# Optimization experiments

Measured on AMD Instinct MI355X. Metric: run time of the kernel, lower is better.

Reference implementation:

```python
import jax, jax.numpy as jnp
import numpy as np

N = 50000; E = 1600000; F = 128; H = 128; C = 40; G = 4
GRID = jnp.linspace(-2.0, 2.0, G)          # FastKAN default grid [-2, 2]
DENOM = 4.0 / (G - 1)                      # (grid_max - grid_min) / (num_grids - 1)
EPS = 1e-5
DIMS = [(F, H), (H, H), (F + 2 * H, C)]    # conv0, conv1, conv_out (skip concat)


def setup_inputs() -> dict:
    key = jax.random.key(0)
    ks = iter(jax.random.split(key, 64))
    inp = {}
    inp["x"] = jax.random.normal(next(ks), (N, F), jnp.float32)
    inp["edge_index"] = jax.random.randint(next(ks), (2, E), 0, N)
    for i, (di, do) in enumerate(DIMS):
        inp[f"c{i}_ln_g"] = jnp.ones((di,), jnp.float32)
        inp[f"c{i}_ln_b"] = jnp.zeros((di,), jnp.float32)
        inp[f"c{i}_sw"] = jax.random.normal(next(ks), (do, di * G), jnp.float32) * 0.1
        inp[f"c{i}_sb"] = jnp.zeros((do,), jnp.float32)
        inp[f"c{i}_bw"] = jax.random.normal(next(ks), (do, di), jnp.float32) * (1.0 / np.sqrt(di))
        inp[f"c{i}_bb"] = jnp.zeros((do,), jnp.float32)
        inp[f"c{i}_bias"] = jnp.zeros((do,), jnp.float32)   # GCNConv output bias
    inp["bn_g"] = jnp.ones((H,), jnp.float32)
    inp["bn_b"] = jnp.zeros((H,), jnp.float32)
    return inp


def _fkan(h, lg, lb, sw, sb, bw, bb):
    # FastKANLayer: LayerNorm -> RBF basis -> spline linear, plus SiLU base branch
    mu = h.mean(-1, keepdims=True)
    var = jnp.mean(jnp.square(h - mu), -1, keepdims=True)
    hn = (h - mu) * jax.lax.rsqrt(var + EPS) * lg + lb
    basis = jnp.exp(-jnp.square((hn[..., None] - GRID) / DENOM))  # [N, d, G]
    basis = basis.reshape(h.shape[0], -1)                          # [N, d*G]
    return basis @ sw.T + sb + jax.nn.silu(h) @ bw.T + bb


def _forward(x, edge_index, params, bn_g, bn_b):
    # gcn_norm with self-loops, symmetric normalization
    row = jnp.concatenate([edge_index[0], jnp.arange(N)])
    col = jnp.concatenate([edge_index[1], jnp.arange(N)])
    deg = jax.ops.segment_sum(jnp.ones_like(row, jnp.float32), col, num_segments=N)
    dis = jnp.where(deg > 0, jax.lax.rsqrt(jnp.maximum(deg, 1e-12)), 0.0)
    norm = dis[row] * dis[col]

    def conv(h, p):
        hw = _fkan(h, *p[:6])  # lin = FKANLayer applied before propagate
        return jax.ops.segment_sum(norm[:, None] * hw[row], col, num_segments=N) + p[6]

    def bn(h):  # BatchNorm1d, training-mode batch stats (biased var); dropout p=0
        mu = h.mean(0)
        var = jnp.mean(jnp.square(h - mu), 0)
        return (h - mu) * jax.lax.rsqrt(var + EPS) * bn_g + bn_b

    skips = [x]
    h = x
    for p in params[:-1]:
        h = bn(conv(h, p))
        skips.append(h)
    h = jnp.concatenate(skips, axis=1)  # skip=True
    return conv(h, params[-1])


def reference(x, edge_index, c0_ln_g, c0_ln_b, c0_sw, c0_sb, c0_bw, c0_bb, c0_bias,
              c1_ln_g, c1_ln_b, c1_sw, c1_sb, c1_bw, c1_bb, c1_bias,
              c2_ln_g, c2_ln_b, c2_sw, c2_sb, c2_bw, c2_bb, c2_bias, bn_g, bn_b):
    params = [
        (c0_ln_g, c0_ln_b, c0_sw, c0_sb, c0_bw, c0_bb, c0_bias),
        (c1_ln_g, c1_ln_b, c1_sw, c1_sb, c1_bw, c1_bb, c1_bias),
        (c2_ln_g, c2_ln_b, c2_sw, c2_sb, c2_bw, c2_bb, c2_bias),
    ]
    return _forward(x, edge_index, params, bn_g, bn_b)
```

## Files before the change

kernel.cpp:

```cpp
#include <hip/hip_runtime.h>
#include <math.h>

constexpr int NN = 50000;
constexpr int NE = 1600000;
constexpr float LN_EPS = 1e-5f;

constexpr int NBKT  = 8;
constexpr int SPAN  = NN / NBKT;
constexpr int CHUNK = 8192;
constexpr int NB1   = (NE + CHUNK - 1) / CHUNK;
constexpr int NSB   = (NN + 255) / 256;

typedef __attribute__((ext_vector_type(8))) short short8;
typedef __attribute__((ext_vector_type(4))) float f32x4;

__device__ __forceinline__ short f2bf(float f)
{
    unsigned u = __builtin_bit_cast(unsigned, f);
    u += 0x7fffu + ((u >> 16) & 1u);
    return (short)(u >> 16);
}

__device__ __forceinline__ float2 bf2x2(unsigned p)
{
    float2 r;
    r.x = __builtin_bit_cast(float, p << 16);
    r.y = __builtin_bit_cast(float, p & 0xffff0000u);
    return r;
}

__global__ __launch_bounds__(256) void csr_hist(const int* __restrict__ col,
                                                int* __restrict__ degi,
                                                int* __restrict__ histo)
{
    __shared__ int hcnt[NBKT];
    const int tid = threadIdx.x;
    if (tid < NBKT) hcnt[tid] = 0;
    __syncthreads();
    const int e0 = blockIdx.x * CHUNK;
    const int e1 = min(e0 + CHUNK, NE);
    for (int e = e0 + tid; e < e1; e += 256) {
        int c = col[e];
        atomicAdd(&degi[c], 1);
        atomicAdd(&hcnt[(unsigned)c / (unsigned)SPAN], 1);
    }
    __syncthreads();
    if (tid < NBKT) histo[tid * NB1 + blockIdx.x] = hcnt[tid];
}

__global__ __launch_bounds__(256) void csr_scan2(int* __restrict__ histo)
{
    constexpr int M = NBKT * NB1;
    constexpr int T = (M + 255) / 256;
    __shared__ int part[256];
    const int t = threadIdx.x;
    int v[T];
    int s = 0;
    #pragma unroll
    for (int j = 0; j < T; ++j) {
        int i = t * T + j;
        v[j] = (i < M) ? histo[i] : 0;
        s += v[j];
    }
    part[t] = s;
    __syncthreads();
    for (int d = 1; d < 256; d <<= 1) {
        int add = (t >= d) ? part[t - d] : 0;
        __syncthreads();
        part[t] += add;
        __syncthreads();
    }
    int run = part[t] - s;
    #pragma unroll
    for (int j = 0; j < T; ++j) {
        int i = t * T + j;
        if (i < M) { histo[i] = run; run += v[j]; }
    }
}

__global__ __launch_bounds__(256) void csr_part(const int* __restrict__ ei,
                                                const int* __restrict__ histo,
                                                uint2* __restrict__ staging)
{
    __shared__ int lcur[NBKT];
    const int tid = threadIdx.x;
    if (tid < NBKT) lcur[tid] = histo[tid * NB1 + blockIdx.x];
    __syncthreads();
    const int e0 = blockIdx.x * CHUNK;
    const int e1 = min(e0 + CHUNK, NE);
    for (int e = e0 + tid; e < e1; e += 256) {
        int r = ei[e];
        int c = ei[NE + e];
        int slot = atomicAdd(&lcur[(unsigned)c / (unsigned)SPAN], 1);
        staging[slot] = make_uint2((unsigned)r, (unsigned)c);
    }
}

template<int PB2>
__global__ __launch_bounds__(256) void csr_scatter(const uint2* __restrict__ staging,
                                                   const int* __restrict__ off,
                                                   int* __restrict__ cur,
                                                   int* __restrict__ rows)
{
    const int b   = blockIdx.x & (NBKT - 1);
    const int blk = blockIdx.x >> 3;
    const int base = off[b * SPAN];
    const int end  = off[(b + 1) * SPAN];
    for (int i = base + blk * 256 + threadIdx.x; i < end; i += PB2 * 256) {
        uint2 e = staging[i];
        int p = off[e.y] + atomicAdd(&cur[e.y], 1);
        rows[p] = (int)e.x;
    }
}

__global__ void dis_kernel(const int* __restrict__ degi, float* __restrict__ dis)
{
    int i = blockIdx.x * 256 + threadIdx.x;
    if (i < NN) dis[i] = rsqrtf((float)degi[i] + 1.0f);
}

__global__ __launch_bounds__(256) void scan_p1(const int* __restrict__ deg,
                                               int* __restrict__ off,
                                               int* __restrict__ partials)
{
    __shared__ int sh[256];
    const int t = threadIdx.x;
    const int i = blockIdx.x * 256 + t;
    int v = (i < NN) ? deg[i] : 0;
    sh[t] = v;
    __syncthreads();
    for (int d = 1; d < 256; d <<= 1) {
        int add = (t >= d) ? sh[t - d] : 0;
        __syncthreads();
        sh[t] += add;
        __syncthreads();
    }
    if (i < NN) off[i] = sh[t] - v;
    if (t == 255) partials[blockIdx.x] = sh[255];
}

__global__ __launch_bounds__(256) void scan_p2(int* __restrict__ partials)
{
    __shared__ int sh[256];
    const int t = threadIdx.x;
    int v = (t < NSB) ? partials[t] : 0;
    sh[t] = v;
    __syncthreads();
    for (int d = 1; d < 256; d <<= 1) {
        int add = (t >= d) ? sh[t - d] : 0;
        __syncthreads();
        sh[t] += add;
        __syncthreads();
    }
    if (t < NSB) partials[t] = sh[t] - v;
    if (t == 255) partials[NSB] = sh[255];
}

__global__ __launch_bounds__(256) void scan_p3(int* __restrict__ off,
                                               const int* __restrict__ partials)
{
    const int i = blockIdx.x * 256 + threadIdx.x;
    if (i < NN) off[i] += partials[blockIdx.x];
    if (i == 0) off[NN] = partials[NSB];
}

__global__ void pack_frag(const float* __restrict__ sw, const float* __restrict__ bw,
                          short* __restrict__ wtf, int D, int OT, int DO, int total)
{
    int idx = blockIdx.x * 256 + threadIdx.x;
    if (idx >= total) return;
    int j8   = idx & 7;
    int lane = (idx >> 3) & 63;
    int rest = idx >> 9;
    int ot = rest % OT, kk = rest / OT;
    int g4 = lane >> 4;
    int s  = kk * 8 + j8;
    int f  = g4 * (D / 4) + s / 5;
    int g5 = s % 5;
    int o  = ot * 16 + (lane & 15);
    float val = 0.f;
    if (o < DO) val = (g5 < 4) ? sw[o * D * 4 + f * 4 + g5] : bw[o * D + f];
    wtf[idx] = f2bf(val);
}

template<int D, int DO, int OT, int KKC, int NODES>
__global__ __launch_bounds__(NODES * 4) void fkan_reg(
    const float* __restrict__ s0, const float* __restrict__ s1, const float* __restrict__ s2,
    const float* __restrict__ ln_g, const float* __restrict__ ln_b,
    const short* __restrict__ wtf, const float* __restrict__ sb, const float* __restrict__ bb,
    short* __restrict__ out)
{
    constexpr int BW  = D / 4;
    constexpr int GBS = BW + 1;
    constexpr int RS  = 4 * GBS + 1;
    __shared__ unsigned pkL[NODES * RS];

    const int tid = threadIdx.x;

    {
        const int anode = tid >> 2, q = tid & 3;
        const int gnode = blockIdx.x * NODES + anode;
        const int snode = (gnode < NN) ? gnode : (NN - 1);
        unsigned* prow = &pkL[anode * RS + q * GBS];
        float sum = 0.f, sq = 0.f;
        #pragma unroll
        for (int i4 = 0; i4 < BW / 4; ++i4) {
            int f = q * BW + i4 * 4;
            const float* src = (D == 128) ? s0 : ((f < 128) ? s0 : (f < 256) ? s1 : s2);
            float4 v = *(const float4*)&src[snode * 128 + (f & 127)];
            sum += (v.x + v.y) + (v.z + v.w);
            sq  += (v.x * v.x + v.y * v.y) + (v.z * v.z + v.w * v.w);
            prow[i4 * 4 + 0] = __builtin_bit_cast(unsigned, v.x);
            prow[i4 * 4 + 1] = __builtin_bit_cast(unsigned, v.y);
            prow[i4 * 4 + 2] = __builtin_bit_cast(unsigned, v.z);
            prow[i4 * 4 + 3] = __builtin_bit_cast(unsigned, v.w);
        }
        sum += __shfl_xor(sum, 1); sum += __shfl_xor(sum, 2);
        sq  += __shfl_xor(sq, 1);  sq  += __shfl_xor(sq, 2);
        float mu   = sum * (1.0f / D);
        float var  = sq * (1.0f / D) - mu * mu;
        float rstd = rsqrtf(var + LN_EPS);
        #pragma unroll 4
        for (int i = 0; i < BW; ++i) {
            int f = q * BW + i;
            float v  = __builtin_bit_cast(float, prow[i]);
            float hn = (v - mu) * rstd * ln_g[f] + ln_b[f];
            float sl = v / (1.0f + __expf(-v));
            prow[i] = ((unsigned)(unsigned short)f2bf(hn) << 16)
                    | ((unsigned)(unsigned short)f2bf(sl) & 0xffffu);
        }
    }
    __syncthreads();

    const int wv = tid >> 6, lane = tid & 63;
    const int m = lane & 15, g4 = lane >> 4;
    const unsigned* pkb = &pkL[(wv * 16 + m) * RS + g4 * GBS];

    f32x4 acc[OT];
    #pragma unroll
    for (int ot = 0; ot < OT; ++ot) acc[ot] = f32x4{0.f, 0.f, 0.f, 0.f};

    union AU { unsigned u[4]; short8 s; };

    for (int per = 0; per < KKC / 5; ++per) {
        const unsigned* pp = pkb + per * 8;
        const short* bp = wtf + ((per * 5) * OT * 512) + lane * 8;
        #pragma unroll
        for (int c = 0; c < 5; ++c) {
            unsigned p[3];
            float h75[3];
            constexpr int FL0[5] = {0, 1, 3, 4, 6};
            constexpr int NF[5]  = {2, 3, 2, 3, 2};
            #pragma unroll
            for (int i = 0; i < 3; ++i) {
                if (i < NF[c]) {
                    p[i] = pp[FL0[c] + i];
                    h75[i] = __builtin_bit_cast(float, p[i] & 0xffff0000u) * 0.75f;
                }
            }
            AU a;
            #pragma unroll
            for (int i = 0; i < 4; ++i) {
                unsigned v2[2];
                #pragma unroll
                for (int h = 0; h < 2; ++h) {
                    int sl = c * 8 + 2 * i + h;
                    int fl = sl / 5 - FL0[c];
                    int g  = sl % 5;
                    if (g == 4) {
                        v2[h] = p[fl] & 0xffffu;
                    } else {
                        float t = h75[fl] + (1.5f - (float)g);
                        float e = __expf(-t * t);
                        v2[h] = (unsigned)(unsigned short)f2bf(e);
                    }
                }
                a.u[i] = (v2[0] & 0xffffu) | (v2[1] << 16);
            }
            #pragma unroll
            for (int ot = 0; ot < OT; ++ot) {
                short8 b = *(const short8*)(bp + (c * OT + ot) * 512);
                acc[ot] = __builtin_amdgcn_mfma_f32_16x16x32_bf16(a.s, b, acc[ot], 0, 0, 0);
            }
        }
    }

    const int nrow0 = blockIdx.x * NODES + wv * 16 + g4 * 4;
    #pragma unroll
    for (int ot = 0; ot < OT; ++ot) {
        int o = ot * 16 + m;
        if (o < DO) {
            float cb = sb[o] + bb[o];
            #pragma unroll
            for (int r = 0; r < 4; ++r) {
                int nr = nrow0 + r;
                if (nr < NN) out[nr * DO + o] = f2bf(acc[ot][r] + cb);
            }
        }
    }
}

template<int DO>
__global__ __launch_bounds__(64) void agg_gather_bf16(
    const int* __restrict__ off, const int* __restrict__ rows,
    const float* __restrict__ dis, const short* __restrict__ hwb,
    const float* __restrict__ bias, float* __restrict__ out)
{
    constexpr int ACT = DO / 2;
    const int n   = blockIdx.x;
    const int tid = threadIdx.x;
    __shared__ int   srow[64];
    __shared__ float swgt[64];

    const int e0 = off[n], e1 = off[n + 1];
    const float dn = dis[n];
    float ax = 0.f, ay = 0.f;
    if (tid < ACT) {
        unsigned p = *(const unsigned*)&hwb[n * DO + 2 * tid];
        float2 v = bf2x2(p);
        ax = dn * dn * v.x + bias[2 * tid];
        ay = dn * dn * v.y + bias[2 * tid + 1];
    }

    for (int t0 = e0; t0 < e1; t0 += 64) {
        const int nt = min(64, e1 - t0);
        if (tid < nt) {
            int r = rows[t0 + tid];
            srow[tid] = r;
            swgt[tid] = dn * dis[r];
        }
        __syncthreads();
        if (tid < ACT) {
            #pragma unroll 4
            for (int j = 0; j < nt; ++j) {
                unsigned p = *(const unsigned*)&hwb[srow[j] * DO + 2 * tid];
                float2 v = bf2x2(p);
                float w = swgt[j];
                ax += w * v.x;
                ay += w * v.y;
            }
        }
        __syncthreads();
    }
    if (tid < ACT) {
        out[n * DO + 2 * tid]     = ax;
        out[n * DO + 2 * tid + 1] = ay;
    }
}

__global__ void bn_stats(const float* __restrict__ h, float* __restrict__ stats)
{
    __shared__ float s1[256], s2[256];
    int c = threadIdx.x & 127;
    int half = threadIdx.x >> 7;
    float sum = 0.f, sq = 0.f;
    for (int n = blockIdx.x * 2 + half; n < NN; n += 512) {
        float v = h[n * 128 + c];
        sum += v; sq += v * v;
    }
    s1[threadIdx.x] = sum; s2[threadIdx.x] = sq;
    __syncthreads();
    if (half == 0) {
        s1[c] += s1[c + 128]; s2[c] += s2[c + 128];
        atomicAdd(&stats[c],        s1[c]);
        atomicAdd(&stats[c + 128],  s2[c]);
    }
}

__global__ void bn_apply(float* __restrict__ h, const float* __restrict__ stats,
                         const float* __restrict__ g, const float* __restrict__ b)
{
    int idx = blockIdx.x * 256 + threadIdx.x;
    if (idx >= NN * 128) return;
    int c = idx & 127;
    float mu  = stats[c] * (1.0f / NN);
    float var = stats[c + 128] * (1.0f / NN) - mu * mu;
    h[idx] = (h[idx] - mu) * rsqrtf(var + LN_EPS) * g[c] + b[c];
}

extern "C" void kernel_launch(void* const* d_in, const int* in_sizes, int n_in,
                              void* d_out, int out_size, void* d_ws, size_t ws_size,
                              hipStream_t stream)
{
    auto F = [&](int i) { return (const float*)d_in[i]; };
    const float* x  = F(0);
    const int*   ei = (const int*)d_in[1];
    const float* bn_g = F(23);
    const float* bn_b = F(24);

    short* wtf0 = (short*)d_ws;
    short* wtf1 = wtf0 + 81920;
    short* wtf2 = wtf1 + 81920;
    short* hwb  = wtf2 + 92160;
    float* dis  = (float*)(hwb + 6400000);
    float* h1   = dis + 50000;
    float* h2   = h1  + 6400000;
    float* stats = h2 + 6400000;
    int*   degi = (int*)(stats + 256);
    int*   off  = degi + 50000;
    int*   cur  = off + 50001;
    int*   rows = cur + 50000;
    int*   histo = rows + NE;
    int*   partials = histo + NBKT * NB1;
    uint2* staging = (uint2*)h1;
    float* outf = (float*)d_out;

    (void)hipMemsetAsync(degi, 0, 50000 * sizeof(int), stream);
    (void)hipMemsetAsync(cur,  0, 50000 * sizeof(int), stream);
    csr_hist<<<NB1, 256, 0, stream>>>(ei + NE, degi, histo);
    dis_kernel<<<(NN + 255) / 256, 256, 0, stream>>>(degi, dis);
    scan_p1<<<NSB, 256, 0, stream>>>(degi, off, partials);
    scan_p2<<<1, 256, 0, stream>>>(partials);
    scan_p3<<<NSB, 256, 0, stream>>>(off, partials);
    csr_scan2<<<1, 256, 0, stream>>>(histo);
    csr_part<<<NB1, 256, 0, stream>>>(ei, histo, staging);
    csr_scatter<128><<<128 * NBKT, 256, 0, stream>>>(staging, off, cur, rows);

    pack_frag<<<(81920 + 255) / 256, 256, 0, stream>>>(F(4),  F(6),  wtf0, 128, 8, 128, 81920);
    pack_frag<<<(81920 + 255) / 256, 256, 0, stream>>>(F(11), F(13), wtf1, 128, 8, 128, 81920);
    pack_frag<<<(92160 + 255) / 256, 256, 0, stream>>>(F(18), F(20), wtf2, 384, 3, 40,  92160);

    const int gridN64 = (NN + 63) / 64;
    const int gridN32 = (NN + 31) / 32;
    const int gridNF  = (NN * 128 + 255) / 256;

    fkan_reg<128, 128, 8, 20, 64><<<gridN64, 256, 0, stream>>>(x, nullptr, nullptr,
        F(2), F(3), wtf0, F(5), F(7), hwb);
    agg_gather_bf16<128><<<NN, 64, 0, stream>>>(off, rows, dis, hwb, F(8), h1);
    (void)hipMemsetAsync(stats, 0, 256 * sizeof(float), stream);
    bn_stats<<<256, 256, 0, stream>>>(h1, stats);
    bn_apply<<<gridNF, 256, 0, stream>>>(h1, stats, bn_g, bn_b);

    fkan_reg<128, 128, 8, 20, 64><<<gridN64, 256, 0, stream>>>(h1, nullptr, nullptr,
        F(9), F(10), wtf1, F(12), F(14), hwb);
    agg_gather_bf16<128><<<NN, 64, 0, stream>>>(off, rows, dis, hwb, F(15), h2);
    (void)hipMemsetAsync(stats, 0, 256 * sizeof(float), stream);
    bn_stats<<<256, 256, 0, stream>>>(h2, stats);
    bn_apply<<<gridNF, 256, 0, stream>>>(h2, stats, bn_g, bn_b);

    fkan_reg<384, 40, 3, 60, 32><<<gridN32, 128, 0, stream>>>(x, h1, h2,
        F(16), F(17), wtf2, F(19), F(21), hwb);
    agg_gather_bf16<40><<<NN, 64, 0, stream>>>(off, rows, dis, hwb, F(22), outf);
}
```

Baseline: 595.6 us.

## Chunk fkan_reg feature staging into LDS to shrink shared memory footprint

The fused LayerNorm/RBF/MFMA kernel now computes LayerNorm statistics in a first pass over global memory. It then stages packed bf16 features into shared memory in NCH chunks, with the last layer using two chunks so the LDS buffer is about half the size. The aim is higher occupancy for the D=384 layer. The cost is reading each input row twice from global memory and an extra block barrier per chunk, and ln_g/ln_b are now loaded as float4.

```diff
diff --git a/kernel.cpp b/kernel.cpp
--- a/kernel.cpp
+++ b/kernel.cpp
@@ -183,58 +183,43 @@
     wtf[idx] = f2bf(val);
 }
 
-template<int D, int DO, int OT, int KKC, int NODES>
+template<int D, int DO, int OT, int KKC, int NODES, int NCH>
 __global__ __launch_bounds__(NODES * 4) void fkan_reg(
     const float* __restrict__ s0, const float* __restrict__ s1, const float* __restrict__ s2,
     const float* __restrict__ ln_g, const float* __restrict__ ln_b,
     const short* __restrict__ wtf, const float* __restrict__ sb, const float* __restrict__ bb,
     short* __restrict__ out)
 {
-    constexpr int BW  = D / 4;
-    constexpr int GBS = BW + 1;
-    constexpr int RS  = 4 * GBS + 1;
+    constexpr int BW   = D / 4;
+    constexpr int CW   = BW / NCH;
+    constexpr int GBS  = CW + 1;
+    constexpr int RS   = 4 * GBS + 1;
+    constexpr int PPC  = (KKC / NCH) / 5;
     __shared__ unsigned pkL[NODES * RS];
 
     const int tid = threadIdx.x;
-
-    {
-        const int anode = tid >> 2, q = tid & 3;
-        const int gnode = blockIdx.x * NODES + anode;
-        const int snode = (gnode < NN) ? gnode : (NN - 1);
-        unsigned* prow = &pkL[anode * RS + q * GBS];
-        float sum = 0.f, sq = 0.f;
-        #pragma unroll
-        for (int i4 = 0; i4 < BW / 4; ++i4) {
-            int f = q * BW + i4 * 4;
-            const float* src = (D == 128) ? s0 : ((f < 128) ? s0 : (f < 256) ? s1 : s2);
-            float4 v = *(const float4*)&src[snode * 128 + (f & 127)];
-            sum += (v.x + v.y) + (v.z + v.w);
-            sq  += (v.x * v.x + v.y * v.y) + (v.z * v.z + v.w * v.w);
-            prow[i4 * 4 + 0] = __builtin_bit_cast(unsigned, v.x);
-            prow[i4 * 4 + 1] = __builtin_bit_cast(unsigned, v.y);
-            prow[i4 * 4 + 2] = __builtin_bit_cast(unsigned, v.z);
-            prow[i4 * 4 + 3] = __builtin_bit_cast(unsigned, v.w);
-        }
-        sum += __shfl_xor(sum, 1); sum += __shfl_xor(sum, 2);
-        sq  += __shfl_xor(sq, 1);  sq  += __shfl_xor(sq, 2);
-        float mu   = sum * (1.0f / D);
-        float var  = sq * (1.0f / D) - mu * mu;
-        float rstd = rsqrtf(var + LN_EPS);
-        #pragma unroll 4
-        for (int i = 0; i < BW; ++i) {
-            int f = q * BW + i;
-            float v  = __builtin_bit_cast(float, prow[i]);
-            float hn = (v - mu) * rstd * ln_g[f] + ln_b[f];
-            float sl = v / (1.0f + __expf(-v));
-            prow[i] = ((unsigned)(unsigned short)f2bf(hn) << 16)
-                    | ((unsigned)(unsigned short)f2bf(sl) & 0xffffu);
-        }
-    }
-    __syncthreads();
+    const int anode = tid >> 2, q = tid & 3;
+    const int gnode = blockIdx.x * NODES + anode;
+    const int snode = (gnode < NN) ? gnode : (NN - 1);
+
+    float sum = 0.f, sq = 0.f;
+    #pragma unroll
+    for (int i4 = 0; i4 < BW / 4; ++i4) {
+        int f = q * BW + i4 * 4;
+        const float* src = (D == 128) ? s0 : ((f < 128) ? s0 : (f < 256) ? s1 : s2);
+        float4 v = *(const float4*)&src[snode * 128 + (f & 127)];
+        sum += (v.x + v.y) + (v.z + v.w);
+        sq  += (v.x * v.x + v.y * v.y) + (v.z * v.z + v.w * v.w);
+    }
+    sum += __shfl_xor(sum, 1); sum += __shfl_xor(sum, 2);
+    sq  += __shfl_xor(sq, 1);  sq  += __shfl_xor(sq, 2);
+    const float mu   = sum * (1.0f / D);
+    const float rstd = rsqrtf(sq * (1.0f / D) - mu * mu + LN_EPS);
 
     const int wv = tid >> 6, lane = tid & 63;
     const int m = lane & 15, g4 = lane >> 4;
     const unsigned* pkb = &pkL[(wv * 16 + m) * RS + g4 * GBS];
+    unsigned* prow = &pkL[anode * RS + q * GBS];
 
     f32x4 acc[OT];
     #pragma unroll
@@ -242,45 +227,72 @@
 
     union AU { unsigned u[4]; short8 s; };
 
-    for (int per = 0; per < KKC / 5; ++per) {
-        const unsigned* pp = pkb + per * 8;
-        const short* bp = wtf + ((per * 5) * OT * 512) + lane * 8;
+    for (int ch = 0; ch < NCH; ++ch) {
+        if (ch) __syncthreads();
         #pragma unroll
-        for (int c = 0; c < 5; ++c) {
-            unsigned p[3];
-            float h75[3];
-            constexpr int FL0[5] = {0, 1, 3, 4, 6};
-            constexpr int NF[5]  = {2, 3, 2, 3, 2};
+        for (int i4 = 0; i4 < CW / 4; ++i4) {
+            int f = q * BW + ch * CW + i4 * 4;
+            const float* src = (D == 128) ? s0 : ((f < 128) ? s0 : (f < 256) ? s1 : s2);
+            float4 v  = *(const float4*)&src[snode * 128 + (f & 127)];
+            float4 lg = *(const float4*)&ln_g[f];
+            float4 lb = *(const float4*)&ln_b[f];
+            float hn[4], sl[4];
+            hn[0] = (v.x - mu) * rstd * lg.x + lb.x;
+            hn[1] = (v.y - mu) * rstd * lg.y + lb.y;
+            hn[2] = (v.z - mu) * rstd * lg.z + lb.z;
+            hn[3] = (v.w - mu) * rstd * lg.w + lb.w;
+            sl[0] = v.x / (1.0f + __expf(-v.x));
+            sl[1] = v.y / (1.0f + __expf(-v.y));
+            sl[2] = v.z / (1.0f + __expf(-v.z));
+            sl[3] = v.w / (1.0f + __expf(-v.w));
             #pragma unroll
-            for (int i = 0; i < 3; ++i) {
-                if (i < NF[c]) {
-                    p[i] = pp[FL0[c] + i];
-                    h75[i] = __builtin_bit_cast(float, p[i] & 0xffff0000u) * 0.75f;
-                }
-            }
-            AU a;
+            for (int k = 0; k < 4; ++k)
+                prow[i4 * 4 + k] = ((unsigned)(unsigned short)f2bf(hn[k]) << 16)
+                                 | ((unsigned)(unsigned short)f2bf(sl[k]) & 0xffffu);
+        }
+        __syncthreads();
+
+        for (int pl = 0; pl < PPC; ++pl) {
+            const unsigned* pp = pkb + pl * 8;
+            const int gper = ch * PPC + pl;
+            const short* bp = wtf + (gper * 5) * OT * 512 + lane * 8;
             #pragma unroll
-            for (int i = 0; i < 4; ++i) {
-                unsigned v2[2];
+            for (int c = 0; c < 5; ++c) {
+                constexpr int FL0[5] = {0, 1, 3, 4, 6};
+                constexpr int NF[5]  = {2, 3, 2, 3, 2};
+                unsigned p[3];
+                float h75[3];
                 #pragma unroll
-                for (int h = 0; h < 2; ++h) {
-                    int sl = c * 8 + 2 * i + h;
-                    int fl = sl / 5 - FL0[c];
-                    int g  = sl % 5;
-                    if (g == 4) {
-                        v2[h] = p[fl] & 0xffffu;
-                    } else {
-                        float t = h75[fl] + (1.5f - (float)g);
-                        float e = __expf(-t * t);
-                        v2[h] = (unsigned)(unsigned short)f2bf(e);
+                for (int i = 0; i < 3; ++i) {
+                    if (i < NF[c]) {
+                        p[i]   = pp[FL0[c] + i];
+                        h75[i] = __builtin_bit_cast(float, p[i] & 0xffff0000u) * 0.75f;
                     }
                 }
-                a.u[i] = (v2[0] & 0xffffu) | (v2[1] << 16);
-            }
-            #pragma unroll
-            for (int ot = 0; ot < OT; ++ot) {
-                short8 b = *(const short8*)(bp + (c * OT + ot) * 512);
-                acc[ot] = __builtin_amdgcn_mfma_f32_16x16x32_bf16(a.s, b, acc[ot], 0, 0, 0);
+                AU a;
+                #pragma unroll
+                for (int i = 0; i < 4; ++i) {
+                    unsigned v2[2];
+                    #pragma unroll
+                    for (int h = 0; h < 2; ++h) {
+                        int sl = c * 8 + 2 * i + h;
+                        int fl = sl / 5 - FL0[c];
+                        int g  = sl % 5;
+                        if (g == 4) {
+                            v2[h] = p[fl] & 0xffffu;
+                        } else {
+                            float t = h75[fl] + (1.5f - (float)g);
+                            float e = __expf(-t * t);
+                            v2[h] = (unsigned)(unsigned short)f2bf(e);
+                        }
+                    }
+                    a.u[i] = (v2[0] & 0xffffu) | (v2[1] << 16);
+                }
+                #pragma unroll
+                for (int ot = 0; ot < OT; ++ot) {
+                    short8 b = *(const short8*)(bp + (c * OT + ot) * 512);
+                    acc[ot] = __builtin_amdgcn_mfma_f32_16x16x32_bf16(a.s, b, acc[ot], 0, 0, 0);
+                }
             }
         }
     }
@@ -424,21 +436,21 @@
     const int gridN32 = (NN + 31) / 32;
     const int gridNF  = (NN * 128 + 255) / 256;
 
-    fkan_reg<128, 128, 8, 20, 64><<<gridN64, 256, 0, stream>>>(x, nullptr, nullptr,
+    fkan_reg<128, 128, 8, 20, 64, 1><<<gridN64, 256, 0, stream>>>(x, nullptr, nullptr,
         F(2), F(3), wtf0, F(5), F(7), hwb);
     agg_gather_bf16<128><<<NN, 64, 0, stream>>>(off, rows, dis, hwb, F(8), h1);
     (void)hipMemsetAsync(stats, 0, 256 * sizeof(float), stream);
     bn_stats<<<256, 256, 0, stream>>>(h1, stats);
     bn_apply<<<gridNF, 256, 0, stream>>>(h1, stats, bn_g, bn_b);
 
-    fkan_reg<128, 128, 8, 20, 64><<<gridN64, 256, 0, stream>>>(h1, nullptr, nullptr,
+    fkan_reg<128, 128, 8, 20, 64, 1><<<gridN64, 256, 0, stream>>>(h1, nullptr, nullptr,
         F(9), F(10), wtf1, F(12), F(14), hwb);
     agg_gather_bf16<128><<<NN, 64, 0, stream>>>(off, rows, dis, hwb, F(15), h2);
     (void)hipMemsetAsync(stats, 0, 256 * sizeof(float), stream);
     bn_stats<<<256, 256, 0, stream>>>(h2, stats);
     bn_apply<<<gridNF, 256, 0, stream>>>(h2, stats, bn_g, bn_b);
 
-    fkan_reg<384, 40, 3, 60, 32><<<gridN32, 128, 0, stream>>>(x, h1, h2,
+    fkan_reg<384, 40, 3, 60, 32, 2><<<gridN32, 128, 0, stream>>>(x, h1, h2,
         F(16), F(17), wtf2, F(19), F(21), hwb);
     agg_gather_bf16<40><<<NN, 64, 0, stream>>>(off, rows, dis, hwb, F(22), outf);
 }
```

Measured after the change: 704.1 us. +18.2%, slower.
